# Performance work log

Measured on AMD Instinct MI355X. Metric: run time of the kernel, lower is better.

## Reference

```python
import jax, jax.numpy as jnp
import numpy as np

H = 512  # hidden_size
IN = 512  # input_size


def setup_inputs() -> dict:
    key = jax.random.key(0)
    ks = jax.random.split(key, 11)
    s = 1.0 / np.sqrt(H)
    T, B = 512, 256
    return {
        "x": jax.random.normal(ks[0], (T, B, IN), jnp.float32),
        "h0": jnp.zeros((B, H), jnp.float32),
        "g0": jnp.zeros((B, H), jnp.float32),
        # torch nn.Linear convention: y = x @ W.T + b, W ~ U(-1/sqrt(fan_in), ..)
        "Wx": jax.random.uniform(ks[1], (4 * H, IN), jnp.float32, -s, s),
        "bx": jax.random.uniform(ks[2], (4 * H,), jnp.float32, -s, s),
        "Wh": jax.random.uniform(ks[3], (3 * H, H), jnp.float32, -s, s),
        "bh": jax.random.uniform(ks[4], (3 * H,), jnp.float32, -s, s),
        "Wgh": jax.random.uniform(ks[5], (3 * H, H), jnp.float32, -s, s),
        "bgh": jax.random.uniform(ks[6], (3 * H,), jnp.float32, -s, s),
        "Whd": jax.random.uniform(ks[7], (3 * H, H), jnp.float32, -s, s),
        "bhd": jax.random.uniform(ks[8], (3 * H,), jnp.float32, -s, s),
        "Wg": jax.random.uniform(ks[9], (2 * H, H), jnp.float32, -s, s),
        "bg": jax.random.uniform(ks[10], (2 * H,), jnp.float32, -s, s),
    }


def _split(a, n):
    return jnp.split(a, n, axis=-1)


def reference(x, h0, g0, Wx, bx, Wh, bh, Wgh, bgh, Whd, bhd, Wg, bg):
    def step(carry, x_t):
        h, g = carry
        x_z, x_r, x_h, x_u = _split(x_t @ Wx.T + bx, 4)
        h_z, h_r, h_u = _split(h @ Wh.T + bh, 3)
        g_z, g_r, g_u = _split(g @ Wgh.T + bgh, 3)
        z = jax.nn.sigmoid(x_z + h_z + g_z)
        r = jax.nn.sigmoid(x_r + h_r + g_r)
        u = jax.nn.sigmoid(x_u + h_u + g_u)
        h_new = (1 - z) * h + z * jnp.tanh(x_h + r * h + u * g)
        h_d = h_new - h
        g_z2, g_r2 = _split(g @ Wg.T + bg, 2)
        hd_z, hd_r, hd_g = _split(h_d @ Whd.T + bhd, 3)
        z2 = jax.nn.sigmoid(hd_z + g_z2)
        r2 = jax.nn.sigmoid(hd_r + g_r2)
        g_new = (1 - z2) * g + z2 * jnp.tanh(hd_g + r2 * g)
        return (h_new, g_new), h_new

    (h, g), hs = jax.lax.scan(step, (h0, g0), x)
    return hs, h[None], g[None]
```

## Files before the change

### kernel.cpp

```cpp
#include <hip/hip_runtime.h>

#define Tn 512
#define Bn 256
#define Hn 512
#define INn 512
#define TPB 512

typedef __attribute__((ext_vector_type(8))) short bf16x8;
typedef __attribute__((ext_vector_type(4))) float f32x4;

__device__ __forceinline__ unsigned short f2bf(float f) {
  unsigned int u = __float_as_uint(f);
  unsigned int r = (u + 0x7fffu + ((u >> 16) & 1u)) >> 16;
  return (unsigned short)r;
}
__device__ __forceinline__ float bf2f(unsigned short u) {
  return __uint_as_float(((unsigned int)u) << 16);
}

__device__ __forceinline__ float sigm(float x) { return 1.0f / (1.0f + __expf(-x)); }
__device__ __forceinline__ float tanh_f(float x) { return 2.0f / (1.0f + __expf(-2.0f * x)) - 1.0f; }

__device__ __forceinline__ bf16x8 ld8(const unsigned short* p) {
  return *reinterpret_cast<const bf16x8*>(p);
}

__device__ __forceinline__ unsigned long long ald8(const unsigned short* p) {
  return __hip_atomic_load((const unsigned long long*)p, __ATOMIC_RELAXED,
                           __HIP_MEMORY_SCOPE_AGENT);
}
__device__ __forceinline__ void ast4(unsigned short* p, unsigned int v) {
  __hip_atomic_store((unsigned int*)p, v, __ATOMIC_RELAXED, __HIP_MEMORY_SCOPE_AGENT);
}

__device__ __forceinline__ f32x4 mfma16(bf16x8 a, bf16x8 b, f32x4 c) {
  return __builtin_amdgcn_mfma_f32_16x16x32_bf16(a, b, c, 0, 0, 0);
}

__global__ __launch_bounds__(256) void cvt_kernel(const float* __restrict__ in,
                                                  unsigned short* __restrict__ out, int n) {
  const int stride = gridDim.x * blockDim.x * 4;
  for (int i = (blockIdx.x * blockDim.x + threadIdx.x) * 4; i < n; i += stride) {
    float4 v = *reinterpret_cast<const float4*>(in + i);
    ushort4 o;
    o.x = f2bf(v.x); o.y = f2bf(v.y); o.z = f2bf(v.z); o.w = f2bf(v.w);
    *reinterpret_cast<ushort4*>(out + i) = o;
  }
}

__global__ __launch_bounds__(256) void xp_gemm_kernel(
    const unsigned short* __restrict__ xb,
    const unsigned short* __restrict__ Wxb,
    const float* __restrict__ bx,
    const float* __restrict__ bh,
    const float* __restrict__ bgh,
    unsigned short* __restrict__ XPb) {
  const int m0 = blockIdx.x * 64;
  const int n0 = blockIdx.y * 64;
  const int wave = threadIdx.x >> 6;
  const int lane = threadIdx.x & 63;
  const int l15 = lane & 15;
  const int lk = (lane >> 4) * 8;
  const int ro = (wave >> 1) * 32;
  const int co = (wave & 1) * 32;
  const unsigned short* ap = xb + (size_t)(m0 + ro + l15) * INn + lk;
  const unsigned short* bp = Wxb + (size_t)(n0 + co + l15) * INn + lk;
  f32x4 acc[2][2] = {};
  for (int k = 0; k < INn; k += 32) {
    bf16x8 a0 = ld8(ap + k);
    bf16x8 a1 = ld8(ap + 16 * INn + k);
    bf16x8 w0 = ld8(bp + k);
    bf16x8 w1 = ld8(bp + 16 * INn + k);
    acc[0][0] = mfma16(a0, w0, acc[0][0]);
    acc[0][1] = mfma16(a0, w1, acc[0][1]);
    acc[1][0] = mfma16(a1, w0, acc[1][0]);
    acc[1][1] = mfma16(a1, w1, acc[1][1]);
  }
#pragma unroll
  for (int rt = 0; rt < 2; ++rt)
#pragma unroll
    for (int ct = 0; ct < 2; ++ct) {
      const int col = n0 + co + ct * 16 + l15;
      const int gate = col >> 9, jcol = col & 511;
      const int jb = jcol >> 4, jl = jcol & 15;
      float bias = bx[col];
      if (col < 1024) bias += bh[col] + bgh[col];
      else if (col >= 1536) bias += bh[col - 512] + bgh[col - 512];
#pragma unroll
      for (int r = 0; r < 4; ++r) {
        const int row = m0 + ro + rt * 16 + (lane >> 4) * 4 + r;
        const int ttl = row >> 8, bb = row & 255;
        XPb[(((size_t)ttl * 8 + (bb >> 5)) * 32 + jb) * 2048 +
            gate * 512 + (bb & 31) * 16 + jl] = f2bf(acc[rt][ct][r] + bias);
      }
    }
}

__device__ __forceinline__ void group_barrier(unsigned int* gflags, int jblk,
                                              unsigned int epoch) {
  __syncthreads();
  if (threadIdx.x < 64) {
    if (threadIdx.x == 0)
      __hip_atomic_store(gflags + jblk, epoch, __ATOMIC_RELAXED,
                         __HIP_MEMORY_SCOPE_AGENT);
    unsigned int* p = gflags + (threadIdx.x & 31);
    while (__hip_atomic_load(p, __ATOMIC_RELAXED, __HIP_MEMORY_SCOPE_AGENT) < epoch)
      __builtin_amdgcn_s_sleep(1);
  }
  __syncthreads();
}

__device__ __forceinline__ void stage_A_part(const unsigned short* src,
                                             unsigned short* dst_l, int b0,
                                             int idx0, int stride, int nIter) {
  for (int q = 0; q < nIter; ++q) {
    const int idx = idx0 + q * stride;
    if (idx < 2048) {
      const int rr = idx >> 6, c = idx & 63;
      union { unsigned long long u[2]; uint4 v; } t;
      const unsigned short* s = src + (size_t)(b0 + rr) * Hn + c * 8;
      t.u[0] = ald8(s);
      t.u[1] = ald8(s + 4);
      *reinterpret_cast<uint4*>(reinterpret_cast<char*>(dst_l) + rr * 1024 +
                                ((c * 16) ^ ((rr & 7) << 4))) = t.v;
    }
  }
}

__global__ __launch_bounds__(512, 2) void persist_kernel(
    const unsigned short* __restrict__ Whb,
    const unsigned short* __restrict__ Wghb,
    const unsigned short* __restrict__ Whdb,
    const unsigned short* __restrict__ Wgb,
    const unsigned short* __restrict__ XPb,
    const float* __restrict__ bhd,
    const float* __restrict__ bg,
    unsigned short* __restrict__ hb0,
    unsigned short* __restrict__ gb,
    unsigned short* __restrict__ hdb,
    float* __restrict__ g_master,
    const float* __restrict__ h0,
    const float* __restrict__ g0,
    float* __restrict__ hs,
    float* __restrict__ h_tail,
    float* __restrict__ g_tail,
    unsigned int* __restrict__ flags,
    int t0, int Tc) {
  __shared__ unsigned short Wh_l[48 * 512];
  __shared__ unsigned short Wgh_l[48 * 512];
  __shared__ unsigned short As_l[32 * 512];
  __shared__ float pa[8][32][17];
  __shared__ unsigned short xp_ls[2][2048];

  const int tid = threadIdx.x;
  const int grp = blockIdx.x & 7;
  const int jblk = blockIdx.x >> 3;
  const int j0 = jblk * 16;
  const int b0 = grp * 32;
  const int wv = tid >> 6;
  const int lane = tid & 63;
  const int l15 = lane & 15;
  const int lk = (lane >> 4) * 8;
  unsigned int* gflags = flags + grp * 32;

  for (int i = tid; i < 48 * 64; i += TPB) {
    const int rr = i >> 6, c = i & 63;
    const int grow = (rr >> 4) * 512 + j0 + (rr & 15);
    const int byte = rr * 1024 + ((c * 16) ^ ((rr & 7) << 4));
    *reinterpret_cast<uint4*>(reinterpret_cast<char*>(Wh_l) + byte) =
        *reinterpret_cast<const uint4*>(Whb + (size_t)grow * 512 + c * 8);
    *reinterpret_cast<uint4*>(reinterpret_cast<char*>(Wgh_l) + byte) =
        *reinterpret_cast<const uint4*>(Wghb + (size_t)grow * 512 + c * 8);
  }

  const int bl_e = tid >> 4, jl_e = tid & 15;
  const int j_e = j0 + jl_e;
  const size_t o_e = (size_t)(b0 + bl_e) * Hn + j_e;
  float h_m = (t0 == 0) ? h0[o_e] : hs[(size_t)(t0 - 1) * (Bn * Hn) + o_e];
  float g_m = (t0 == 0) ? g0[o_e] : g_master[o_e];
  const float bz2 = bhd[j_e] + bg[j_e];
  const float br2 = bhd[512 + j_e] + bg[512 + j_e];
  const float bgc = bhd[1024 + j_e];
  const int xo = bl_e * 16 + jl_e;

  {
    const unsigned short* src = XPb + ((size_t)grp * 32 + jblk) * 2048;
    *(unsigned long long*)&xp_ls[0][tid * 4] =
        *(const unsigned long long*)(src + tid * 4);
  }

  unsigned long long rA[16][2][2];
  if (wv == 0) {
    const unsigned short* ap0 =
        hb0 + (size_t)(t0 & 1) * (Bn * Hn) + (size_t)(b0 + l15) * Hn + lk;
#pragma unroll
    for (int kt = 0; kt < 16; ++kt) {
      rA[kt][0][0] = ald8(ap0 + kt * 32);
      rA[kt][0][1] = ald8(ap0 + kt * 32 + 4);
      rA[kt][1][0] = ald8(ap0 + 16 * Hn + kt * 32);
      rA[kt][1][1] = ald8(ap0 + 16 * Hn + kt * 32 + 4);
    }
  }
  __syncthreads();

  unsigned int epoch = 0;
  float z2p = 0.0f, r2p = 0.0f;
  const int swzA = (l15 & 7) << 4;

  for (int tt = 0; tt < Tc; ++tt) {
    const int t = t0 + tt;
    unsigned short* hb_nxt = hb0 + (size_t)((t + 1) & 1) * (Bn * Hn);
    const int cur = tt & 1, nxt = (tt + 1) & 1;

    if (wv >= 1) {
      stage_A_part(gb, As_l, b0, tid - 64, 448, 5);
      if (wv >= 3 && tt + 1 < Tc) {
        const unsigned short* src =
            XPb + (((size_t)(tt + 1) * 8 + grp) * 32 + jblk) * 2048;
        for (int i = tid - 192; i < 512; i += 320)
          *(unsigned long long*)&xp_ls[nxt][i * 4] =
              *(const unsigned long long*)(src + i * 4);
      }
    }
    __syncthreads();

    if (wv == 0) {
      f32x4 acc[2][3] = {};
#pragma unroll
      for (int kt = 0; kt < 16; ++kt) {
        union { unsigned long long u[2]; bf16x8 v; } a0, a1;
        a0.u[0] = rA[kt][0][0]; a0.u[1] = rA[kt][0][1];
        a1.u[0] = rA[kt][1][0]; a1.u[1] = rA[kt][1][1];
        const int k = kt * 32;
#pragma unroll
        for (int s = 0; s < 3; ++s) {
          const int rr = s * 16 + l15;
          const int byte = rr * 1024 + (((k + lk) * 2) ^ swzA);
          bf16x8 bw = *reinterpret_cast<const bf16x8*>(
              reinterpret_cast<const char*>(Wh_l) + byte);
          acc[0][s] = mfma16(a0.v, bw, acc[0][s]);
          acc[1][s] = mfma16(a1.v, bw, acc[1][s]);
        }
      }
#pragma unroll
      for (int s = 0; s < 3; ++s)
#pragma unroll
        for (int rt = 0; rt < 2; ++rt)
#pragma unroll
          for (int r = 0; r < 4; ++r)
            pa[s][rt * 16 + (lane >> 4) * 4 + r][l15] = acc[rt][s][r];
    } else if (wv == 1) {
      f32x4 acc[2][3] = {};
#pragma unroll
      for (int kt = 0; kt < 16; ++kt) {
        const int k = kt * 32;
        const int abyte = ((k + lk) * 2) ^ swzA;
        bf16x8 a0 = *reinterpret_cast<const bf16x8*>(
            reinterpret_cast<const char*>(As_l) + l15 * 1024 + abyte);
        bf16x8 a1 = *reinterpret_cast<const bf16x8*>(
            reinterpret_cast<const char*>(As_l) + (16 + l15) * 1024 + abyte);
#pragma unroll
        for (int s = 0; s < 3; ++s) {
          const int rr = s * 16 + l15;
          const int byte = rr * 1024 + (((k + lk) * 2) ^ swzA);
          bf16x8 bw = *reinterpret_cast<const bf16x8*>(
              reinterpret_cast<const char*>(Wgh_l) + byte);
          acc[0][s] = mfma16(a0, bw, acc[0][s]);
          acc[1][s] = mfma16(a1, bw, acc[1][s]);
        }
      }
#pragma unroll
      for (int s = 0; s < 3; ++s)
#pragma unroll
        for (int rt = 0; rt < 2; ++rt)
#pragma unroll
          for (int r = 0; r < 4; ++r)
            pa[3 + s][rt * 16 + (lane >> 4) * 4 + r][l15] = acc[rt][s][r];
    } else if (wv == 2) {
      const unsigned short* bp0 = Wgb + (size_t)(j0 + l15) * Hn + lk;
      const unsigned short* bp1 = Wgb + (size_t)(512 + j0 + l15) * Hn + lk;
      f32x4 acc[2][2] = {};
#pragma unroll
      for (int kt = 0; kt < 16; ++kt) {
        const int k = kt * 32;
        const int abyte = ((k + lk) * 2) ^ swzA;
        bf16x8 a0 = *reinterpret_cast<const bf16x8*>(
            reinterpret_cast<const char*>(As_l) + l15 * 1024 + abyte);
        bf16x8 a1 = *reinterpret_cast<const bf16x8*>(
            reinterpret_cast<const char*>(As_l) + (16 + l15) * 1024 + abyte);
        bf16x8 w0 = ld8(bp0 + k);
        bf16x8 w1 = ld8(bp1 + k);
        acc[0][0] = mfma16(a0, w0, acc[0][0]);
        acc[1][0] = mfma16(a1, w0, acc[1][0]);
        acc[0][1] = mfma16(a0, w1, acc[0][1]);
        acc[1][1] = mfma16(a1, w1, acc[1][1]);
      }
#pragma unroll
      for (int s = 0; s < 2; ++s)
#pragma unroll
        for (int rt = 0; rt < 2; ++rt)
#pragma unroll
          for (int r = 0; r < 4; ++r)
            pa[6 + s][rt * 16 + (lane >> 4) * 4 + r][l15] = acc[rt][s][r];
    }
    __syncthreads();

    {
      const float z = sigm(bf2f(xp_ls[cur][xo]) + pa[0][bl_e][jl_e] + pa[3][bl_e][jl_e]);
      const float r = sigm(bf2f(xp_ls[cur][512 + xo]) + pa[1][bl_e][jl_e] + pa[4][bl_e][jl_e]);
      const float u = sigm(bf2f(xp_ls[cur][1536 + xo]) + pa[2][bl_e][jl_e] + pa[5][bl_e][jl_e]);
      const float cand = tanh_f(bf2f(xp_ls[cur][1024 + xo]) + r * h_m + u * g_m);
      const float hn = (1.0f - z) * h_m + z * cand;
      const float hd = hn - h_m;
      hs[(size_t)t * (Bn * Hn) + o_e] = hn;
      if (t == Tn - 1) h_tail[o_e] = hn;
      const unsigned int hn_u = f2bf(hn), hd_u = f2bf(hd);
      const unsigned int hn_hi = (unsigned int)__shfl_down((int)hn_u, 1);
      const unsigned int hd_hi = (unsigned int)__shfl_down((int)hd_u, 1);
      if ((jl_e & 1) == 0) {
        ast4(hb_nxt + o_e, hn_u | (hn_hi << 16));
        ast4(hdb + o_e, hd_u | (hd_hi << 16));
      }
      h_m = hn;
      z2p = pa[6][bl_e][jl_e];
      r2p = pa[7][bl_e][jl_e];
    }
    group_barrier(gflags, jblk, ++epoch);

    stage_A_part(hdb, As_l, b0, tid, 512, 4);
    __syncthreads();

    if (wv < 3) {
      const unsigned short* bp0 = Whdb + (size_t)(wv * 512 + j0 + l15) * Hn + lk;
      f32x4 acc[2] = {};
#pragma unroll
      for (int kt = 0; kt < 16; ++kt) {
        const int k = kt * 32;
        const int abyte = ((k + lk) * 2) ^ swzA;
        bf16x8 a0 = *reinterpret_cast<const bf16x8*>(
            reinterpret_cast<const char*>(As_l) + l15 * 1024 + abyte);
        bf16x8 a1 = *reinterpret_cast<const bf16x8*>(
            reinterpret_cast<const char*>(As_l) + (16 + l15) * 1024 + abyte);
        bf16x8 w0 = ld8(bp0 + k);
        acc[0] = mfma16(a0, w0, acc[0]);
        acc[1] = mfma16(a1, w0, acc[1]);
      }
#pragma unroll
      for (int rt = 0; rt < 2; ++rt)
#pragma unroll
        for (int r = 0; r < 4; ++r)
          pa[wv][rt * 16 + (lane >> 4) * 4 + r][l15] = acc[rt][r];
    }
    if (wv == 0 && tt + 1 < Tc) {
      const unsigned short* ap0 = hb_nxt + (size_t)(b0 + l15) * Hn + lk;
#pragma unroll
      for (int kt = 0; kt < 16; ++kt) {
        rA[kt][0][0] = ald8(ap0 + kt * 32);
        rA[kt][0][1] = ald8(ap0 + kt * 32 + 4);
        rA[kt][1][0] = ald8(ap0 + 16 * Hn + kt * 32);
        rA[kt][1][1] = ald8(ap0 + 16 * Hn + kt * 32 + 4);
      }
    }
    __syncthreads();

    {
      const float z2 = sigm(pa[0][bl_e][jl_e] + z2p + bz2);
      const float r2 = sigm(pa[1][bl_e][jl_e] + r2p + br2);
      const float gc = tanh_f(pa[2][bl_e][jl_e] + bgc + r2 * g_m);
      const float gn = (1.0f - z2) * g_m + z2 * gc;
      g_m = gn;
      if (t == Tn - 1) g_tail[o_e] = gn;
      const unsigned int gn_u = f2bf(gn);
      const unsigned int gn_hi = (unsigned int)__shfl_down((int)gn_u, 1);
      if ((jl_e & 1) == 0) ast4(gb + o_e, gn_u | (gn_hi << 16));
    }
    group_barrier(gflags, jblk, ++epoch);
  }
  g_master[o_e] = g_m;
}

extern "C" void kernel_launch(void* const* d_in, const int* in_sizes, int n_in,
                              void* d_out, int out_size, void* d_ws, size_t ws_size,
                              hipStream_t stream) {
  const float* x   = (const float*)d_in[0];
  const float* h0  = (const float*)d_in[1];
  const float* g0  = (const float*)d_in[2];
  const float* Wx  = (const float*)d_in[3];
  const float* bx  = (const float*)d_in[4];
  const float* Wh  = (const float*)d_in[5];
  const float* bh  = (const float*)d_in[6];
  const float* Wgh = (const float*)d_in[7];
  const float* bgh = (const float*)d_in[8];
  const float* Whd = (const float*)d_in[9];
  const float* bhd = (const float*)d_in[10];
  const float* Wg  = (const float*)d_in[11];
  const float* bg  = (const float*)d_in[12];

  char* ws = (char*)d_ws;
  unsigned short* Whb  = (unsigned short*)(ws + 0);
  unsigned short* Wghb = (unsigned short*)(ws + 1572864);
  unsigned short* Whdb = (unsigned short*)(ws + 3145728);
  unsigned short* Wgb  = (unsigned short*)(ws + 4718592);
  unsigned short* Wxb  = (unsigned short*)(ws + 5767168);
  unsigned short* hb0  = (unsigned short*)(ws + 7864320);
  unsigned short* gb_  = (unsigned short*)(ws + 8388608);
  unsigned short* hdb  = (unsigned short*)(ws + 8650752);
  float* g_master      = (float*)(ws + 8912896);
  unsigned int* flags  = (unsigned int*)(ws + 9437184);
  const size_t FIXED = 9453568ULL;

  int Tc = 64;
  while (Tc > 1 && FIXED + (size_t)Tc * (262144ULL + 1048576ULL) > ws_size) Tc >>= 1;
  unsigned short* xb  = (unsigned short*)(ws + FIXED);
  unsigned short* XPb = (unsigned short*)(ws + FIXED + (size_t)Tc * 262144ULL);

  float* hs = (float*)d_out;
  float* h_tail = hs + (size_t)Tn * Bn * Hn;
  float* g_tail = h_tail + (size_t)Bn * Hn;

  hipMemsetAsync(flags, 0, 16384, stream);
  cvt_kernel<<<dim3(512), 256, 0, stream>>>(Wh, Whb, 1536 * 512);
  cvt_kernel<<<dim3(512), 256, 0, stream>>>(Wgh, Wghb, 1536 * 512);
  cvt_kernel<<<dim3(512), 256, 0, stream>>>(Whd, Whdb, 1536 * 512);
  cvt_kernel<<<dim3(512), 256, 0, stream>>>(Wg, Wgb, 1024 * 512);
  cvt_kernel<<<dim3(512), 256, 0, stream>>>(Wx, Wxb, 2048 * 512);
  cvt_kernel<<<dim3(128), 256, 0, stream>>>(h0, hb0, Bn * Hn);
  cvt_kernel<<<dim3(128), 256, 0, stream>>>(g0, gb_, Bn * Hn);

  const int nChunks = Tn / Tc;
  for (int c = 0; c < nChunks; ++c) {
    const int t0 = c * Tc;
    cvt_kernel<<<dim3(1024), 256, 0, stream>>>(x + (size_t)t0 * Bn * INn, xb,
                                               Tc * Bn * INn);
    xp_gemm_kernel<<<dim3(Tc * 4, 32), 256, 0, stream>>>(xb, Wxb, bx, bh, bgh, XPb);
    persist_kernel<<<dim3(256), dim3(TPB), 0, stream>>>(
        Whb, Wghb, Whdb, Wgb, XPb, bhd, bg, hb0, gb_, hdb, g_master, h0, g0,
        hs, h_tail, g_tail, flags + c * 256, t0, Tc);
  }
}
```

Measured before the change: 9.088 ms.

## Restructure persistent GRU step into two-phase pipeline with separate H/G flag barriers

Reorganizes the persistent recurrent kernel so the h-update and g-update phases each wait on their own per-group flag arrays (FH, FG) instead of a full group barrier. Each phase gathers only the state it needs into two shared A buffers, and the g-dependent GEMMs for the next step run right after g is published. Per-wave work is rebalanced so eight waves each compute one 16-column gate slice. The Wgh weights now stream from global memory instead of LDS, and launch bounds drop to one block per CU. The intent is to shorten the serialized critical path and barrier cost per timestep, at the cost of more global weight traffic and trickier cross-block flag ordering.

```diff
diff --git a/kernel.cpp b/kernel.cpp
--- a/kernel.cpp
+++ b/kernel.cpp
@@ -31,6 +31,12 @@
 }
 __device__ __forceinline__ void ast4(unsigned short* p, unsigned int v) {
   __hip_atomic_store((unsigned int*)p, v, __ATOMIC_RELAXED, __HIP_MEMORY_SCOPE_AGENT);
+}
+__device__ __forceinline__ unsigned int aldf(const unsigned int* p) {
+  return __hip_atomic_load(p, __ATOMIC_RELAXED, __HIP_MEMORY_SCOPE_AGENT);
+}
+__device__ __forceinline__ void astf(unsigned int* p, unsigned int v) {
+  __hip_atomic_store(p, v, __ATOMIC_RELAXED, __HIP_MEMORY_SCOPE_AGENT);
 }
 
 __device__ __forceinline__ f32x4 mfma16(bf16x8 a, bf16x8 b, f32x4 c) {
@@ -96,38 +102,35 @@
     }
 }
 
-__device__ __forceinline__ void group_barrier(unsigned int* gflags, int jblk,
-                                              unsigned int epoch) {
-  __syncthreads();
-  if (threadIdx.x < 64) {
-    if (threadIdx.x == 0)
-      __hip_atomic_store(gflags + jblk, epoch, __ATOMIC_RELAXED,
-                         __HIP_MEMORY_SCOPE_AGENT);
-    unsigned int* p = gflags + (threadIdx.x & 31);
-    while (__hip_atomic_load(p, __ATOMIC_RELAXED, __HIP_MEMORY_SCOPE_AGENT) < epoch)
-      __builtin_amdgcn_s_sleep(1);
-  }
-  __syncthreads();
-}
-
-__device__ __forceinline__ void stage_A_part(const unsigned short* src,
-                                             unsigned short* dst_l, int b0,
-                                             int idx0, int stride, int nIter) {
-  for (int q = 0; q < nIter; ++q) {
-    const int idx = idx0 + q * stride;
-    if (idx < 2048) {
-      const int rr = idx >> 6, c = idx & 63;
-      union { unsigned long long u[2]; uint4 v; } t;
-      const unsigned short* s = src + (size_t)(b0 + rr) * Hn + c * 8;
-      t.u[0] = ald8(s);
-      t.u[1] = ald8(s + 4);
-      *reinterpret_cast<uint4*>(reinterpret_cast<char*>(dst_l) + rr * 1024 +
-                                ((c * 16) ^ ((rr & 7) << 4))) = t.v;
-    }
-  }
-}
-
-__global__ __launch_bounds__(512, 2) void persist_kernel(
+__device__ __forceinline__ void poll_flags(const unsigned int* f, unsigned int ep,
+                                           int jblk) {
+  const int lane = threadIdx.x & 63;
+  const int w = threadIdx.x >> 6;
+  const int src = (w << 2) + ((lane & 7) >> 1);
+  if (src == jblk) return;
+  const unsigned int* p = f + src;
+  while (aldf(p) < ep) __builtin_amdgcn_s_sleep(1);
+}
+
+__device__ __forceinline__ void gather32(const unsigned short* src,
+                                         unsigned short* dst, int b0) {
+  const int lane = threadIdx.x & 63;
+  const int w = threadIdx.x >> 6;
+  const int c = (w << 3) + (lane & 7);
+  const int r0 = (lane >> 3) << 2;
+#pragma unroll
+  for (int p = 0; p < 4; ++p) {
+    const int rr = r0 + p;
+    const unsigned short* s = src + (size_t)(b0 + rr) * Hn + c * 8;
+    unsigned long long lo = ald8(s);
+    unsigned long long hi = ald8(s + 4);
+    char* d = (char*)dst + rr * 1024 + ((c * 16) ^ ((rr & 7) << 4));
+    *(unsigned long long*)d = lo;
+    *(unsigned long long*)(d + 8) = hi;
+  }
+}
+
+__global__ __launch_bounds__(512, 1) void persist_kernel(
     const unsigned short* __restrict__ Whb,
     const unsigned short* __restrict__ Wghb,
     const unsigned short* __restrict__ Whdb,
@@ -144,11 +147,11 @@
     float* __restrict__ hs,
     float* __restrict__ h_tail,
     float* __restrict__ g_tail,
-    unsigned int* __restrict__ flags,
+    unsigned int* __restrict__ slab,
     int t0, int Tc) {
   __shared__ unsigned short Wh_l[48 * 512];
-  __shared__ unsigned short Wgh_l[48 * 512];
-  __shared__ unsigned short As_l[32 * 512];
+  __shared__ unsigned short As_h[32 * 512];
+  __shared__ unsigned short As_B[32 * 512];
   __shared__ float pa[8][32][17];
   __shared__ unsigned short xp_ls[2][2048];
 
@@ -161,7 +164,8 @@
   const int lane = tid & 63;
   const int l15 = lane & 15;
   const int lk = (lane >> 4) * 8;
-  unsigned int* gflags = flags + grp * 32;
+  unsigned int* FH = slab + grp * 64;
+  unsigned int* FG = slab + grp * 64 + 32;
 
   for (int i = tid; i < 48 * 64; i += TPB) {
     const int rr = i >> 6, c = i & 63;
@@ -169,8 +173,11 @@
     const int byte = rr * 1024 + ((c * 16) ^ ((rr & 7) << 4));
     *reinterpret_cast<uint4*>(reinterpret_cast<char*>(Wh_l) + byte) =
         *reinterpret_cast<const uint4*>(Whb + (size_t)grow * 512 + c * 8);
-    *reinterpret_cast<uint4*>(reinterpret_cast<char*>(Wgh_l) + byte) =
-        *reinterpret_cast<const uint4*>(Wghb + (size_t)grow * 512 + c * 8);
+  }
+  {
+    const unsigned short* src = XPb + ((size_t)grp * 32 + jblk) * 2048;
+    *(unsigned long long*)&xp_ls[0][tid * 4] =
+        *(const unsigned long long*)(src + tid * 4);
   }
 
   const int bl_e = tid >> 4, jl_e = tid & 15;
@@ -182,191 +189,124 @@
   const float br2 = bhd[512 + j_e] + bg[512 + j_e];
   const float bgc = bhd[1024 + j_e];
   const int xo = bl_e * 16 + jl_e;
-
+  const int swzA = (l15 & 7) << 4;
+  float z2p = 0.0f, r2p = 0.0f;
+
+  gather32(hb0 + (size_t)(t0 & 1) * (Bn * Hn), As_h, b0);
+  gather32(gb, As_B, b0);
+  __syncthreads();
   {
-    const unsigned short* src = XPb + ((size_t)grp * 32 + jblk) * 2048;
-    *(unsigned long long*)&xp_ls[0][tid * 4] =
-        *(const unsigned long long*)(src + tid * 4);
-  }
-
-  unsigned long long rA[16][2][2];
-  if (wv == 0) {
-    const unsigned short* ap0 =
-        hb0 + (size_t)(t0 & 1) * (Bn * Hn) + (size_t)(b0 + l15) * Hn + lk;
+    const unsigned short* As = (wv < 3) ? As_h : As_B;
+    const unsigned short* bp =
+        (wv < 3) ? nullptr
+        : (wv < 6) ? Wghb + (size_t)((wv - 3) * 512 + j0 + l15) * Hn + lk
+                   : Wgb + (size_t)((wv - 6) * 512 + j0 + l15) * Hn + lk;
+    const int wrow = wv * 16 + l15;
+    f32x4 acc0 = {}, acc1 = {};
 #pragma unroll
     for (int kt = 0; kt < 16; ++kt) {
-      rA[kt][0][0] = ald8(ap0 + kt * 32);
-      rA[kt][0][1] = ald8(ap0 + kt * 32 + 4);
-      rA[kt][1][0] = ald8(ap0 + 16 * Hn + kt * 32);
-      rA[kt][1][1] = ald8(ap0 + 16 * Hn + kt * 32 + 4);
+      const int k2 = (kt * 32 + lk) * 2;
+      const int abyte = k2 ^ swzA;
+      bf16x8 a0 = *reinterpret_cast<const bf16x8*>(
+          reinterpret_cast<const char*>(As) + l15 * 1024 + abyte);
+      bf16x8 a1 = *reinterpret_cast<const bf16x8*>(
+          reinterpret_cast<const char*>(As) + (16 + l15) * 1024 + abyte);
+      bf16x8 bw = (wv < 3)
+          ? *reinterpret_cast<const bf16x8*>(
+                reinterpret_cast<const char*>(Wh_l) + wrow * 1024 + (k2 ^ ((wrow & 7) << 4)))
+          : ld8(bp + kt * 32);
+      acc0 = mfma16(a0, bw, acc0);
+      acc1 = mfma16(a1, bw, acc1);
+    }
+#pragma unroll
+    for (int r = 0; r < 4; ++r) {
+      pa[wv][(lane >> 4) * 4 + r][l15] = acc0[r];
+      pa[wv][16 + (lane >> 4) * 4 + r][l15] = acc1[r];
     }
   }
   __syncthreads();
-
-  unsigned int epoch = 0;
-  float z2p = 0.0f, r2p = 0.0f;
-  const int swzA = (l15 & 7) << 4;
+  {
+    const float z = sigm(bf2f(xp_ls[0][xo]) + pa[0][bl_e][jl_e] + pa[3][bl_e][jl_e]);
+    const float r = sigm(bf2f(xp_ls[0][512 + xo]) + pa[1][bl_e][jl_e] + pa[4][bl_e][jl_e]);
+    const float u = sigm(bf2f(xp_ls[0][1536 + xo]) + pa[2][bl_e][jl_e] + pa[5][bl_e][jl_e]);
+    const float cand = tanh_f(bf2f(xp_ls[0][1024 + xo]) + r * h_m + u * g_m);
+    const float hn = (1.0f - z) * h_m + z * cand;
+    const float hd = hn - h_m;
+    hs[(size_t)t0 * (Bn * Hn) + o_e] = hn;
+    const unsigned int hn_u = f2bf(hn), hd_u = f2bf(hd);
+    const unsigned int hn_hi = (unsigned int)__shfl_down((int)hn_u, 1);
+    const unsigned int hd_hi = (unsigned int)__shfl_down((int)hd_u, 1);
+    if ((jl_e & 1) == 0) {
+      ast4(hb0 + (size_t)((t0 + 1) & 1) * (Bn * Hn) + o_e, hn_u | (hn_hi << 16));
+      ast4(hdb + o_e, hd_u | (hd_hi << 16));
+    }
+    z2p = pa[6][bl_e][jl_e];
+    r2p = pa[7][bl_e][jl_e];
+    h_m = hn;
+  }
+  __syncthreads();
+  if (tid == 0) astf(FH + jblk, 1u);
 
   for (int tt = 0; tt < Tc; ++tt) {
     const int t = t0 + tt;
-    unsigned short* hb_nxt = hb0 + (size_t)((t + 1) & 1) * (Bn * Hn);
-    const int cur = tt & 1, nxt = (tt + 1) & 1;
-
-    if (wv >= 1) {
-      stage_A_part(gb, As_l, b0, tid - 64, 448, 5);
-      if (wv >= 3 && tt + 1 < Tc) {
-        const unsigned short* src =
-            XPb + (((size_t)(tt + 1) * 8 + grp) * 32 + jblk) * 2048;
-        for (int i = tid - 192; i < 512; i += 320)
-          *(unsigned long long*)&xp_ls[nxt][i * 4] =
-              *(const unsigned long long*)(src + i * 4);
-      }
-    }
-    __syncthreads();
-
-    if (wv == 0) {
-      f32x4 acc[2][3] = {};
+
+    poll_flags(FH, (unsigned int)(tt + 1), jblk);
+    gather32(hb0 + (size_t)((t + 1) & 1) * (Bn * Hn), As_h, b0);
+    gather32(hdb, As_B, b0);
+    __syncthreads();
+    if (wv < 3) {
+      const int wrow = wv * 16 + l15;
+      f32x4 acc0 = {}, acc1 = {};
 #pragma unroll
       for (int kt = 0; kt < 16; ++kt) {
-        union { unsigned long long u[2]; bf16x8 v; } a0, a1;
-        a0.u[0] = rA[kt][0][0]; a0.u[1] = rA[kt][0][1];
-        a1.u[0] = rA[kt][1][0]; a1.u[1] = rA[kt][1][1];
-        const int k = kt * 32;
-#pragma unroll
-        for (int s = 0; s < 3; ++s) {
-          const int rr = s * 16 + l15;
-          const int byte = rr * 1024 + (((k + lk) * 2) ^ swzA);
-          bf16x8 bw = *reinterpret_cast<const bf16x8*>(
-              reinterpret_cast<const char*>(Wh_l) + byte);
-          acc[0][s] = mfma16(a0.v, bw, acc[0][s]);
-          acc[1][s] = mfma16(a1.v, bw, acc[1][s]);
-        }
-      }
-#pragma unroll
-      for (int s = 0; s < 3; ++s)
-#pragma unroll
-        for (int rt = 0; rt < 2; ++rt)
-#pragma unroll
-          for (int r = 0; r < 4; ++r)
-            pa[s][rt * 16 + (lane >> 4) * 4 + r][l15] = acc[rt][s][r];
-    } else if (wv == 1) {
-      f32x4 acc[2][3] = {};
+        const int k2 = (kt * 32 + lk) * 2;
+        const int abyte = k2 ^ swzA;
+        bf16x8 a0 = *reinterpret_cast<const bf16x8*>(
+            reinterpret_cast<const char*>(As_h) + l15 * 1024 + abyte);
+        bf16x8 a1 = *reinterpret_cast<const bf16x8*>(
+            reinterpret_cast<const char*>(As_h) + (16 + l15) * 1024 + abyte);
+        bf16x8 bw = *reinterpret_cast<const bf16x8*>(
+            reinterpret_cast<const char*>(Wh_l) + wrow * 1024 + (k2 ^ ((wrow & 7) << 4)));
+        acc0 = mfma16(a0, bw, acc0);
+        acc1 = mfma16(a1, bw, acc1);
+      }
+#pragma unroll
+      for (int r = 0; r < 4; ++r) {
+        pa[wv][(lane >> 4) * 4 + r][l15] = acc0[r];
+        pa[wv][16 + (lane >> 4) * 4 + r][l15] = acc1[r];
+      }
+    } else if (wv < 6) {
+      const unsigned short* bp = Whdb + (size_t)((wv - 3) * 512 + j0 + l15) * Hn + lk;
+      f32x4 acc0 = {}, acc1 = {};
 #pragma unroll
       for (int kt = 0; kt < 16; ++kt) {
-        const int k = kt * 32;
-        const int abyte = ((k + lk) * 2) ^ swzA;
+        const int k2 = (kt * 32 + lk) * 2;
+        const int abyte = k2 ^ swzA;
         bf16x8 a0 = *reinterpret_cast<const bf16x8*>(
-            reinterpret_cast<const char*>(As_l) + l15 * 1024 + abyte);
+            reinterpret_cast<const char*>(As_B) + l15 * 1024 + abyte);
         bf16x8 a1 = *reinterpret_cast<const bf16x8*>(
-            reinterpret_cast<const char*>(As_l) + (16 + l15) * 1024 + abyte);
-#pragma unroll
-        for (int s = 0; s < 3; ++s) {
-          const int rr = s * 16 + l15;
-          const int byte = rr * 1024 + (((k + lk) * 2) ^ swzA);
-          bf16x8 bw = *reinterpret_cast<const bf16x8*>(
-              reinterpret_cast<const char*>(Wgh_l) + byte);
-          acc[0][s] = mfma16(a0, bw, acc[0][s]);
-          acc[1][s] = mfma16(a1, bw, acc[1][s]);
-        }
-      }
-#pragma unroll
-      for (int s = 0; s < 3; ++s)
-#pragma unroll
-        for (int rt = 0; rt < 2; ++rt)
-#pragma unroll
-          for (int r = 0; r < 4; ++r)
-            pa[3 + s][rt * 16 + (lane >> 4) * 4 + r][l15] = acc[rt][s][r];
-    } else if (wv == 2) {
-      const unsigned short* bp0 = Wgb + (size_t)(j0 + l15) * Hn + lk;
-      const unsigned short* bp1 = Wgb + (size_t)(512 + j0 + l15) * Hn + lk;
-      f32x4 acc[2][2] = {};
-#pragma unroll
-      for (int kt = 0; kt < 16; ++kt) {
-        const int k = kt * 32;
-        const int abyte = ((k + lk) * 2) ^ swzA;
-        bf16x8 a0 = *reinterpret_cast<const bf16x8*>(
-            reinterpret_cast<const char*>(As_l) + l15 * 1024 + abyte);
-        bf16x8 a1 = *reinterpret_cast<const bf16x8*>(
-            reinterpret_cast<const char*>(As_l) + (16 + l15) * 1024 + abyte);
-        bf16x8 w0 = ld8(bp0 + k);
-        bf16x8 w1 = ld8(bp1 + k);
-        acc[0][0] = mfma16(a0, w0, acc[0][0]);
-        acc[1][0] = mfma16(a1, w0, acc[1][0]);
-        acc[0][1] = mfma16(a0, w1, acc[0][1]);
-        acc[1][1] = mfma16(a1, w1, acc[1][1]);
-      }
-#pragma unroll
-      for (int s = 0; s < 2; ++s)
-#pragma unroll
-        for (int rt = 0; rt < 2; ++rt)
-#pragma unroll
-          for (int r = 0; r < 4; ++r)
-            pa[6 + s][rt * 16 + (lane >> 4) * 4 + r][l15] = acc[rt][s][r];
-    }
-    __syncthreads();
-
+            reinterpret_cast<const char*>(As_B) + (16 + l15) * 1024 + abyte);
+        bf16x8 bw = ld8(bp + kt * 32);
+        acc0 = mfma16(a0, bw, acc0);
+        acc1 = mfma16(a1, bw, acc1);
+      }
+#pragma unroll
+      for (int r = 0; r < 4; ++r) {
+        pa[wv][(lane >> 4) * 4 + r][l15] = acc0[r];
+        pa[wv][16 + (lane >> 4) * 4 + r][l15] = acc1[r];
+      }
+    } else if (tt + 1 < Tc) {
+      const unsigned short* src =
+          XPb + (((size_t)(tt + 1) * 8 + grp) * 32 + jblk) * 2048;
+      for (int i = tid - 384; i < 512; i += 128)
+        *(unsigned long long*)&xp_ls[(tt + 1) & 1][i * 4] =
+            *(const unsigned long long*)(src + i * 4);
+    }
+    __syncthreads();
     {
-      const float z = sigm(bf2f(xp_ls[cur][xo]) + pa[0][bl_e][jl_e] + pa[3][bl_e][jl_e]);
-      const float r = sigm(bf2f(xp_ls[cur][512 + xo]) + pa[1][bl_e][jl_e] + pa[4][bl_e][jl_e]);
-      const float u = sigm(bf2f(xp_ls[cur][1536 + xo]) + pa[2][bl_e][jl_e] + pa[5][bl_e][jl_e]);
-      const float cand = tanh_f(bf2f(xp_ls[cur][1024 + xo]) + r * h_m + u * g_m);
-      const float hn = (1.0f - z) * h_m + z * cand;
-      const float hd = hn - h_m;
-      hs[(size_t)t * (Bn * Hn) + o_e] = hn;
-      if (t == Tn - 1) h_tail[o_e] = hn;
-      const unsigned int hn_u = f2bf(hn), hd_u = f2bf(hd);
-      const unsigned int hn_hi = (unsigned int)__shfl_down((int)hn_u, 1);
-      const unsigned int hd_hi = (unsigned int)__shfl_down((int)hd_u, 1);
-      if ((jl_e & 1) == 0) {
-        ast4(hb_nxt + o_e, hn_u | (hn_hi << 16));
-        ast4(hdb + o_e, hd_u | (hd_hi << 16));
-      }
-      h_m = hn;
-      z2p = pa[6][bl_e][jl_e];
-      r2p = pa[7][bl_e][jl_e];
-    }
-    group_barrier(gflags, jblk, ++epoch);
-
-    stage_A_part(hdb, As_l, b0, tid, 512, 4);
-    __syncthreads();
-
-    if (wv < 3) {
-      const unsigned short* bp0 = Whdb + (size_t)(wv * 512 + j0 + l15) * Hn + lk;
-      f32x4 acc[2] = {};
-#pragma unroll
-      for (int kt = 0; kt < 16; ++kt) {
-        const int k = kt * 32;
-        const int abyte = ((k + lk) * 2) ^ swzA;
-        bf16x8 a0 = *reinterpret_cast<const bf16x8*>(
-            reinterpret_cast<const char*>(As_l) + l15 * 1024 + abyte);
-        bf16x8 a1 = *reinterpret_cast<const bf16x8*>(
-            reinterpret_cast<const char*>(As_l) + (16 + l15) * 1024 + abyte);
-        bf16x8 w0 = ld8(bp0 + k);
-        acc[0] = mfma16(a0, w0, acc[0]);
-        acc[1] = mfma16(a1, w0, acc[1]);
-      }
-#pragma unroll
-      for (int rt = 0; rt < 2; ++rt)
-#pragma unroll
-        for (int r = 0; r < 4; ++r)
-          pa[wv][rt * 16 + (lane >> 4) * 4 + r][l15] = acc[rt][r];
-    }
-    if (wv == 0 && tt + 1 < Tc) {
-      const unsigned short* ap0 = hb_nxt + (size_t)(b0 + l15) * Hn + lk;
-#pragma unroll
-      for (int kt = 0; kt < 16; ++kt) {
-        rA[kt][0][0] = ald8(ap0 + kt * 32);
-        rA[kt][0][1] = ald8(ap0 + kt * 32 + 4);
-        rA[kt][1][0] = ald8(ap0 + 16 * Hn + kt * 32);
-        rA[kt][1][1] = ald8(ap0 + 16 * Hn + kt * 32 + 4);
-      }
-    }
-    __syncthreads();
-
-    {
-      const float z2 = sigm(pa[0][bl_e][jl_e] + z2p + bz2);
-      const float r2 = sigm(pa[1][bl_e][jl_e] + r2p + br2);
-      const float gc = tanh_f(pa[2][bl_e][jl_e] + bgc + r2 * g_m);
+      const float z2 = sigm(pa[3][bl_e][jl_e] + z2p + bz2);
+      const float r2 = sigm(pa[4][bl_e][jl_e] + r2p + br2);
+      const float gc = tanh_f(pa[5][bl_e][jl_e] + bgc + r2 * g_m);
       const float gn = (1.0f - z2) * g_m + z2 * gc;
       g_m = gn;
       if (t == Tn - 1) g_tail[o_e] = gn;
@@ -374,7 +314,61 @@
       const unsigned int gn_hi = (unsigned int)__shfl_down((int)gn_u, 1);
       if ((jl_e & 1) == 0) ast4(gb + o_e, gn_u | (gn_hi << 16));
     }
-    group_barrier(gflags, jblk, ++epoch);
+    __syncthreads();
+    if (tid == 0) astf(FG + jblk, (unsigned int)(tt + 1));
+
+    if (tt + 1 >= Tc) break;
+
+    poll_flags(FG, (unsigned int)(tt + 1), jblk);
+    gather32(gb, As_B, b0);
+    __syncthreads();
+    if (wv < 5) {
+      const unsigned short* bp =
+          (wv < 3) ? Wghb + (size_t)(wv * 512 + j0 + l15) * Hn + lk
+                   : Wgb + (size_t)((wv - 3) * 512 + j0 + l15) * Hn + lk;
+      f32x4 acc0 = {}, acc1 = {};
+#pragma unroll
+      for (int kt = 0; kt < 16; ++kt) {
+        const int k2 = (kt * 32 + lk) * 2;
+        const int abyte = k2 ^ swzA;
+        bf16x8 a0 = *reinterpret_cast<const bf16x8*>(
+            reinterpret_cast<const char*>(As_B) + l15 * 1024 + abyte);
+        bf16x8 a1 = *reinterpret_cast<const bf16x8*>(
+            reinterpret_cast<const char*>(As_B) + (16 + l15) * 1024 + abyte);
+        bf16x8 bw = ld8(bp + kt * 32);
+        acc0 = mfma16(a0, bw, acc0);
+        acc1 = mfma16(a1, bw, acc1);
+      }
+#pragma unroll
+      for (int r = 0; r < 4; ++r) {
+        pa[3 + wv][(lane >> 4) * 4 + r][l15] = acc0[r];
+        pa[3 + wv][16 + (lane >> 4) * 4 + r][l15] = acc1[r];
+      }
+    }
+    __syncthreads();
+    {
+      const int xb_ = (tt + 1) & 1;
+      const float z = sigm(bf2f(xp_ls[xb_][xo]) + pa[0][bl_e][jl_e] + pa[3][bl_e][jl_e]);
+      const float r = sigm(bf2f(xp_ls[xb_][512 + xo]) + pa[1][bl_e][jl_e] + pa[4][bl_e][jl_e]);
+      const float u = sigm(bf2f(xp_ls[xb_][1536 + xo]) + pa[2][bl_e][jl_e] + pa[5][bl_e][jl_e]);
+      const float cand = tanh_f(bf2f(xp_ls[xb_][1024 + xo]) + r * h_m + u * g_m);
+      const float hn = (1.0f - z) * h_m + z * cand;
+      const float hd = hn - h_m;
+      hs[(size_t)(t + 1) * (Bn * Hn) + o_e] = hn;
+      if (t + 1 == Tn - 1) h_tail[o_e] = hn;
+      const unsigned int hn_u = f2bf(hn), hd_u = f2bf(hd);
+      const unsigned int hn_hi = (unsigned int)__shfl_down((int)hn_u, 1);
+      const unsigned int hd_hi = (unsigned int)__shfl_down((int)hd_u, 1);
+      if ((jl_e & 1) == 0) {
+        ast4(hb0 + (size_t)(t & 1) * (Bn * Hn) + o_e, hn_u | (hn_hi << 16));
+        ast4(hdb + o_e, hd_u | (hd_hi << 16));
+      }
+      z2p = pa[6][bl_e][jl_e];
+      r2p = pa[7][bl_e][jl_e];
+      h_m = hn;
+    }
+    __syncthreads();
+    if (tid == 0) astf(FH + jblk, (unsigned int)(tt + 2));
   }
   g_master[o_e] = g_m;
 }
@@ -435,6 +429,6 @@
     xp_gemm_kernel<<<dim3(Tc * 4, 32), 256, 0, stream>>>(xb, Wxb, bx, bh, bgh, XPb);
     persist_kernel<<<dim3(256), dim3(TPB), 0, stream>>>(
         Whb, Wghb, Whdb, Wgb, XPb, bhd, bg, hb0, gb_, hdb, g_master, h0, g0,
-        hs, h_tail, g_tail, flags + c * 256, t0, Tc);
-  }
-}
+        hs, h_tail, g_tail, flags + c * 512, t0, Tc);
+  }
+}
```

New measurement: 9.710 ms. 1.07x slower.
